# Performance work log

Hardware: AMD Instinct MI355X
Metric: run time of the kernel (lower is better)

## Reference

```python
import jax, jax.numpy as jnp
import numpy as np

B, T, C = 4, 2048, 1024
H = 16
D = C // H  # head_size = 64


def setup_inputs() -> dict:
    key = jax.random.key(0)
    ks = jax.random.split(key, 5)
    s = 0.02
    return {
        "x": jax.random.normal(ks[0], (B, T, C), dtype=jnp.float32),
        "Wq": jax.random.normal(ks[1], (C, C), dtype=jnp.float32) * s,
        "Wk": jax.random.normal(ks[2], (C, C), dtype=jnp.float32) * s,
        "Wv": jax.random.normal(ks[3], (C, C), dtype=jnp.float32) * s,
        "Wp": jax.random.normal(ks[4], (C, C), dtype=jnp.float32) * s,
        "bp": jnp.zeros((C,), dtype=jnp.float32),
    }


def reference(x, Wq, Wk, Wv, Wp, bp):
    Bq, Tq, Cq = x.shape
    # torch Linear: y = x @ W.T ; split into heads [B, H, T, D]
    def split(y):
        return y.reshape(Bq, Tq, H, D).transpose(0, 2, 1, 3)
    q = split(x @ Wq.T)
    k = split(x @ Wk.T)
    v = split(x @ Wv.T)
    # NOTE: original scales by C**-0.5 (full n_embed), not head_size**-0.5
    scale = Cq ** (-0.5)
    att = jnp.einsum('bhqd,bhkd->bhqk', q, k) * scale  # [B,H,T,T]
    causal = jnp.tril(jnp.ones((Tq, Tq), dtype=bool))
    att = jnp.where(causal[None, None, :, :], att, -jnp.inf)
    att = jax.nn.softmax(att, axis=-1)
    out = jnp.einsum('bhqk,bhkd->bhqd', att, v)  # [B,H,T,D]
    out = out.transpose(0, 2, 1, 3).reshape(Bq, Tq, Cq)
    return out @ Wp.T + bp
```

## Files before the change

kernel.cpp:

```cpp
#include <hip/hip_runtime.h>
#include <cstdint>
#include <cstddef>

typedef __attribute__((ext_vector_type(8))) __bf16 bf16x8;
typedef __attribute__((ext_vector_type(4))) __bf16 bf16x4;
typedef __attribute__((ext_vector_type(4))) float f32x4;
typedef __attribute__((ext_vector_type(16))) float f32x16;
typedef __attribute__((ext_vector_type(4))) unsigned uint4v;

#define B_ 4
#define T_ 2048
#define C_ 1024
#define H_ 16
#define D_ 64
#define NTILES_ (T_ / 32)
#define TILE_ELEMS_ 2048
#define BH_STRIDE_ ((size_t)NTILES_ * TILE_ELEMS_)

__device__ __forceinline__ float fexp2(float x) {
#if __has_builtin(__builtin_amdgcn_exp2f)
  return __builtin_amdgcn_exp2f(x);
#else
  return __expf(x * 0.69314718f);
#endif
}

__global__ __launch_bounds__(256) void castall(
    const float* __restrict__ x, const float* __restrict__ wq, const float* __restrict__ wk,
    const float* __restrict__ wv, const float* __restrict__ wp,
    __bf16* __restrict__ xb, __bf16* __restrict__ wqb, __bf16* __restrict__ wkb,
    __bf16* __restrict__ wvb, __bf16* __restrict__ wpb) {
  const int bid = blockIdx.x;
  const float* src;
  __bf16* dst;
  if (bid < 8192)       { src = x  + (size_t)bid * 1024;           dst = xb  + (size_t)bid * 1024; }
  else if (bid < 9216)  { src = wq + (size_t)(bid - 8192) * 1024;  dst = wqb + (size_t)(bid - 8192) * 1024; }
  else if (bid < 10240) { src = wk + (size_t)(bid - 9216) * 1024;  dst = wkb + (size_t)(bid - 9216) * 1024; }
  else if (bid < 11264) { src = wv + (size_t)(bid - 10240) * 1024; dst = wvb + (size_t)(bid - 10240) * 1024; }
  else                  { src = wp + (size_t)(bid - 11264) * 1024; dst = wpb + (size_t)(bid - 11264) * 1024; }
  const int i = threadIdx.x * 4;
  float4 f = *reinterpret_cast<const float4*>(src + i);
  bf16x4 o;
  o[0] = (__bf16)f.x; o[1] = (__bf16)f.y; o[2] = (__bf16)f.z; o[3] = (__bf16)f.w;
  *reinterpret_cast<bf16x4*>(dst + i) = o;
}

__device__ __forceinline__ void gload_lds16(const __bf16* g, __bf16* lds) {
  __builtin_amdgcn_global_load_lds(
      (const __attribute__((address_space(1))) void*)g,
      (__attribute__((address_space(3))) void*)lds, 16, 0, 0);
}

template <typename OUTT, bool BIAS>
__device__ __forceinline__ void gemm_bt_body(const __bf16* __restrict__ A,
                                             const __bf16* __restrict__ Bt,
                                             OUTT* __restrict__ Cp,
                                             const float* __restrict__ bias,
                                             int M, int N, int K) {
  constexpr int BK = 64;
  __shared__ __bf16 As[128 * BK];
  __shared__ __bf16 Bs[128 * BK];
  const int tid = threadIdx.x;
  const int w = tid >> 6, l = tid & 63;
  const int wr = w >> 1, wc = w & 1;
  const int lr = l & 15, lg = l >> 4;
  const int m0 = blockIdx.y * 128, n0 = blockIdx.x * 128;
  const int srow = l >> 3, scol = (l & 7) * 8;

  f32x4 acc[4][4] = {};

  for (int k0 = 0; k0 < K; k0 += BK) {
#pragma unroll
    for (int it = 0; it < 4; ++it) {
      const int c = w * 4 + it;
      gload_lds16(A + (size_t)(m0 + 8 * c + srow) * K + k0 + scol, As + c * 512);
      gload_lds16(Bt + (size_t)(n0 + 8 * c + srow) * K + k0 + scol, Bs + c * 512);
    }
    __syncthreads();
    bf16x8 af[4][2], bfv[4][2];
#pragma unroll
    for (int m = 0; m < 4; ++m)
#pragma unroll
      for (int kk = 0; kk < 2; ++kk)
        af[m][kk] = *reinterpret_cast<const bf16x8*>(As + (wr * 64 + m * 16 + lr) * BK + kk * 32 + lg * 8);
#pragma unroll
    for (int n = 0; n < 4; ++n)
#pragma unroll
      for (int kk = 0; kk < 2; ++kk)
        bfv[n][kk] = *reinterpret_cast<const bf16x8*>(Bs + (wc * 64 + n * 16 + lr) * BK + kk * 32 + lg * 8);
#pragma unroll
    for (int kk = 0; kk < 2; ++kk)
#pragma unroll
      for (int m = 0; m < 4; ++m)
#pragma unroll
        for (int n = 0; n < 4; ++n)
          acc[m][n] = __builtin_amdgcn_mfma_f32_16x16x32_bf16(af[m][kk], bfv[n][kk], acc[m][n], 0, 0, 0);
    __syncthreads();
  }
#pragma unroll
  for (int m = 0; m < 4; ++m)
#pragma unroll
    for (int n = 0; n < 4; ++n) {
      const int col = n0 + wc * 64 + n * 16 + lr;
      float bv = 0.f;
      if (BIAS) bv = bias[col];
#pragma unroll
      for (int j = 0; j < 4; ++j) {
        const int row = m0 + wr * 64 + m * 16 + lg * 4 + j;
        Cp[(size_t)row * N + col] = (OUTT)(acc[m][n][j] + bv);
      }
    }
}

__global__ __launch_bounds__(256) void gemm_proj(const __bf16* __restrict__ ao,
    const __bf16* __restrict__ wp, float* __restrict__ out, const float* __restrict__ bp) {
  gemm_bt_body<float, true>(ao, wp, out, bp, B_ * T_, C_, C_);
}

#define STAGE_A(BUFO, KT, HH)                                                         \
  do {                                                                                \
    const __bf16* s0_ = Agp + (size_t)(m0 + (HH) * 128 + srow) * 1024 + (KT) * 64 + sswz; \
    gload_lds16(s0_, LDSb + (BUFO) + (HH) * 8192 + w * 1024);                         \
    gload_lds16(s0_ + 8 * 1024, LDSb + (BUFO) + (HH) * 8192 + w * 1024 + 512);        \
  } while (0)
#define STAGE_B(BUFO, KT, HH)                                                         \
  do {                                                                                \
    const __bf16* s0_ = Bgp + (size_t)(n0 + (HH) * 128 + srow) * 1024 + (KT) * 64 + sswz; \
    gload_lds16(s0_, LDSb + 32768 + (BUFO) + (HH) * 8192 + w * 1024);                 \
    gload_lds16(s0_ + 8 * 1024, LDSb + 32768 + (BUFO) + (HH) * 8192 + w * 1024 + 512);\
  } while (0)
#define RD_A(M, KK) (*reinterpret_cast<const bf16x8*>(                                \
    LDSb + bufo + (wr * 128 + (M) * 16 + lr) * 64 + (((KK) * 32 + lg * 8) ^ ((lr & 7) * 8))))
#define RD_B(N, KK) (*reinterpret_cast<const bf16x8*>(                                \
    LDSb + 32768 + bufo + (wc * 64 + (N) * 16 + lr) * 64 + (((KK) * 32 + lg * 8) ^ ((lr & 7) * 8))))

__global__ __launch_bounds__(512, 2) void gemm_qkv8(
    const __bf16* __restrict__ Agp, const __bf16* __restrict__ Bgp,
    __bf16* __restrict__ qf, __bf16* __restrict__ kf, __bf16* __restrict__ vf) {
  __shared__ __bf16 LDSb[65536];
  const int tid = threadIdx.x;
  const int w = tid >> 6, l = tid & 63;
  const int wr = w >> 2, wc = w & 3;
  const int lr = l & 15, lg = l >> 4;
  int lin = blockIdx.y * 12 + blockIdx.x;
  lin = (lin & 7) * 48 + (lin >> 3);
  const int bx = lin % 12, by = lin / 12;
  const int m0 = by * 256, n0 = bx * 256;
  const int srow = w * 16 + (l >> 3);
  const int sswz = ((l & 7) ^ ((l >> 3) & 7)) * 8;

  f32x4 acc[8][4] = {};
  bf16x8 afl[4][2], bfl[2][2], bfh[2][2];

  STAGE_A(0, 0, 0); STAGE_A(0, 0, 1);
  STAGE_B(0, 0, 0); STAGE_B(0, 0, 1);
  __builtin_amdgcn_sched_barrier(0);
  asm volatile("s_waitcnt vmcnt(0)" ::: "memory");
  __builtin_amdgcn_s_barrier();
  __builtin_amdgcn_sched_barrier(0);

  for (int t = 0; t < 16; ++t) {
    const int bufo = (t & 1) * 16384;
    const int nbo = ((t + 1) & 1) * 16384;
    const bool st = t < 15;
#pragma unroll
    for (int m = 0; m < 4; ++m) { afl[m][0] = RD_A(m, 0); afl[m][1] = RD_A(m, 1); }
    bfl[0][0] = RD_B(0, 0); bfl[0][1] = RD_B(0, 1);
    bfl[1][0] = RD_B(1, 0); bfl[1][1] = RD_B(1, 1);
    if (st) STAGE_A(nbo, t + 1, 0);
    __builtin_amdgcn_s_setprio(1);
#pragma unroll
    for (int kk = 0; kk < 2; ++kk)
#pragma unroll
      for (int m = 0; m < 4; ++m) {
        acc[m][0] = __builtin_amdgcn_mfma_f32_16x16x32_bf16(afl[m][kk], bfl[0][kk], acc[m][0], 0, 0, 0);
        acc[m][1] = __builtin_amdgcn_mfma_f32_16x16x32_bf16(afl[m][kk], bfl[1][kk], acc[m][1], 0, 0, 0);
      }
    __builtin_amdgcn_s_setprio(0);
    __builtin_amdgcn_s_barrier();
    bfh[0][0] = RD_B(2, 0); bfh[0][1] = RD_B(2, 1);
    bfh[1][0] = RD_B(3, 0); bfh[1][1] = RD_B(3, 1);
    if (st) STAGE_A(nbo, t + 1, 1);
    __builtin_amdgcn_s_setprio(1);
#pragma unroll
    for (int kk = 0; kk < 2; ++kk)
#pragma unroll
      for (int m = 0; m < 4; ++m) {
        acc[m][2] = __builtin_amdgcn_mfma_f32_16x16x32_bf16(afl[m][kk], bfh[0][kk], acc[m][2], 0, 0, 0);
        acc[m][3] = __builtin_amdgcn_mfma_f32_16x16x32_bf16(afl[m][kk], bfh[1][kk], acc[m][3], 0, 0, 0);
      }
    __builtin_amdgcn_s_setprio(0);
    __builtin_amdgcn_s_barrier();
#pragma unroll
    for (int m = 0; m < 4; ++m) { afl[m][0] = RD_A(m + 4, 0); afl[m][1] = RD_A(m + 4, 1); }
    if (st) STAGE_B(nbo, t + 1, 0);
    __builtin_amdgcn_s_setprio(1);
#pragma unroll
    for (int kk = 0; kk < 2; ++kk)
#pragma unroll
      for (int m = 0; m < 4; ++m) {
        acc[m + 4][0] = __builtin_amdgcn_mfma_f32_16x16x32_bf16(afl[m][kk], bfl[0][kk], acc[m + 4][0], 0, 0, 0);
        acc[m + 4][1] = __builtin_amdgcn_mfma_f32_16x16x32_bf16(afl[m][kk], bfl[1][kk], acc[m + 4][1], 0, 0, 0);
      }
    __builtin_amdgcn_s_setprio(0);
    __builtin_amdgcn_s_barrier();
    if (st) STAGE_B(nbo, t + 1, 1);
    __builtin_amdgcn_s_setprio(1);
#pragma unroll
    for (int kk = 0; kk < 2; ++kk)
#pragma unroll
      for (int m = 0; m < 4; ++m) {
        acc[m + 4][2] = __builtin_amdgcn_mfma_f32_16x16x32_bf16(afl[m][kk], bfh[0][kk], acc[m + 4][2], 0, 0, 0);
        acc[m + 4][3] = __builtin_amdgcn_mfma_f32_16x16x32_bf16(afl[m][kk], bfh[1][kk], acc[m + 4][3], 0, 0, 0);
      }
    __builtin_amdgcn_s_setprio(0);
    __builtin_amdgcn_sched_barrier(0);
    asm volatile("s_waitcnt vmcnt(0)" ::: "memory");
    __builtin_amdgcn_s_barrier();
    __builtin_amdgcn_sched_barrier(0);
  }

  __bf16* wl = LDSb + w * 8192;
  const int colb = n0 + wc * 64;
  const int mat = colb >> 10;
  const int h = (colb >> 6) & 15;
  const int b = m0 >> 11;
  const float qsc = (mat == 0) ? 0.04508422f : 1.0f;
#pragma unroll
  for (int m = 0; m < 8; ++m) {
    const int rt = m >> 1;
#pragma unroll
    for (int n = 0; n < 4; ++n) {
      const int d = n * 16 + lr;
#pragma unroll
      for (int j = 0; j < 4; ++j) {
        const int rowloc = (m & 1) * 16 + lg * 4 + j;
        int off;
        if (mat < 2)
          off = ((d >> 4) & 3) * 512 + ((d >> 3) & 1) * 256 + rowloc * 8 + (d & 7);
        else
          off = (d >> 5) * 1024 + ((rowloc >> 4) & 1) * 512 + ((rowloc >> 3) & 1) * 256 +
                (d & 31) * 8 + (rowloc & 7);
        wl[rt * 2048 + off] = (__bf16)(acc[m][n][j] * qsc);
      }
    }
  }
  __bf16* dstbase = (mat == 0 ? qf : mat == 1 ? kf : vf) + (size_t)(b * 16 + h) * BH_STRIDE_;
  const int rt0 = ((m0 + wr * 128) >> 5) & 63;
#pragma unroll
  for (int rt = 0; rt < 4; ++rt)
#pragma unroll
    for (int c = 0; c < 4; ++c) {
      const bf16x8 vchunk = *reinterpret_cast<const bf16x8*>(wl + rt * 2048 + c * 512 + l * 8);
      *reinterpret_cast<bf16x8*>(dstbase + (size_t)(rt0 + rt) * TILE_ELEMS_ + c * 512 + l * 8) = vchunk;
    }
}

__device__ __forceinline__ unsigned pk2(float a, float b) {
  const unsigned short ua = __builtin_bit_cast(unsigned short, (__bf16)a);
  const unsigned short ub = __builtin_bit_cast(unsigned short, (__bf16)b);
  return (unsigned)ua | ((unsigned)ub << 16);
}

#define LOADKV(SFX, TT)                                                          \
  do {                                                                           \
    const __bf16* kp_ = kfb + (size_t)(TT) * TILE_ELEMS_ + lx8;                  \
    k##SFX##0 = *reinterpret_cast<const bf16x8*>(kp_);                           \
    k##SFX##1 = *reinterpret_cast<const bf16x8*>(kp_ + 512);                     \
    k##SFX##2 = *reinterpret_cast<const bf16x8*>(kp_ + 1024);                    \
    k##SFX##3 = *reinterpret_cast<const bf16x8*>(kp_ + 1536);                    \
    const __bf16* vp_ = vfb + (size_t)(TT) * TILE_ELEMS_ + lx8;                  \
    v##SFX##0 = *reinterpret_cast<const bf16x8*>(vp_);                           \
    v##SFX##1 = *reinterpret_cast<const bf16x8*>(vp_ + 512);                     \
    v##SFX##2 = *reinterpret_cast<const bf16x8*>(vp_ + 1024);                    \
    v##SFX##3 = *reinterpret_cast<const bf16x8*>(vp_ + 1536);                    \
  } while (0)

#define TILE(SFX, MASKED)                                                        \
  do {                                                                           \
    f32x16 s = {};                                                               \
    __builtin_amdgcn_s_setprio(1);                                               \
    s = __builtin_amdgcn_mfma_f32_32x32x16_bf16(k##SFX##0, qf[0], s, 0, 0, 0);   \
    s = __builtin_amdgcn_mfma_f32_32x32x16_bf16(k##SFX##1, qf[1], s, 0, 0, 0);   \
    s = __builtin_amdgcn_mfma_f32_32x32x16_bf16(k##SFX##2, qf[2], s, 0, 0, 0);   \
    s = __builtin_amdgcn_mfma_f32_32x32x16_bf16(k##SFX##3, qf[3], s, 0, 0, 0);   \
    __builtin_amdgcn_s_setprio(0);                                               \
    float sv[16];                                                                \
    _Pragma("unroll") for (int r = 0; r < 16; ++r) sv[r] = s[r];                 \
    if (MASKED) {                                                                \
      _Pragma("unroll") for (int r = 0; r < 16; ++r) {                           \
        const int kvloc = (r & 3) + 8 * (r >> 2) + 4 * hi;                       \
        sv[r] = (kvloc <= lane31) ? sv[r] : -1e30f;                              \
      }                                                                          \
    }                                                                            \
    _Pragma("unroll") for (int r = 0; r < 16; ++r) sv[r] = fexp2(sv[r]);         \
    unsigned pwv[8];                                                             \
    _Pragma("unroll") for (int ks = 0; ks < 2; ++ks) {                           \
      const unsigned X0 = pk2(sv[ks * 8 + 0], sv[ks * 8 + 1]);                   \
      const unsigned X1 = pk2(sv[ks * 8 + 2], sv[ks * 8 + 3]);                   \
      const unsigned Y0 = pk2(sv[ks * 8 + 4], sv[ks * 8 + 5]);                   \
      const unsigned Y1 = pk2(sv[ks * 8 + 6], sv[ks * 8 + 7]);                   \
      const unsigned sX0 = __shfl_xor(X0, 32);                                   \
      const unsigned sX1 = __shfl_xor(X1, 32);                                   \
      const unsigned sY0 = __shfl_xor(Y0, 32);                                   \
      const unsigned sY1 = __shfl_xor(Y1, 32);                                   \
      pwv[ks * 4 + 0] = hi ? sY0 : X0;                                           \
      pwv[ks * 4 + 1] = hi ? sY1 : X1;                                           \
      pwv[ks * 4 + 2] = hi ? Y0 : sX0;                                           \
      pwv[ks * 4 + 3] = hi ? Y1 : sX1;                                           \
    }                                                                            \
    const uint4v u0 = {pwv[0], pwv[1], pwv[2], pwv[3]};                          \
    const uint4v u1 = {pwv[4], pwv[5], pwv[6], pwv[7]};                          \
    const bf16x8 pf0 = __builtin_bit_cast(bf16x8, u0);                           \
    const bf16x8 pf1 = __builtin_bit_cast(bf16x8, u1);                           \
    __builtin_amdgcn_s_setprio(1);                                               \
    acc0 = __builtin_amdgcn_mfma_f32_32x32x16_bf16(v##SFX##0, pf0, acc0, 0, 0, 0); \
    acc0 = __builtin_amdgcn_mfma_f32_32x32x16_bf16(v##SFX##1, pf1, acc0, 0, 0, 0); \
    acc1 = __builtin_amdgcn_mfma_f32_32x32x16_bf16(v##SFX##2, pf0, acc1, 0, 0, 0); \
    acc1 = __builtin_amdgcn_mfma_f32_32x32x16_bf16(v##SFX##3, pf1, acc1, 0, 0, 0); \
    __builtin_amdgcn_s_setprio(0);                                               \
    float b8[8];                                                                 \
    _Pragma("unroll") for (int r = 0; r < 8; ++r) b8[r] = sv[2 * r] + sv[2 * r + 1]; \
    _Pragma("unroll") for (int r = 0; r < 4; ++r) b8[r] = b8[2 * r] + b8[2 * r + 1]; \
    l_run += (b8[0] + b8[1]) + (b8[2] + b8[3]);                                  \
  } while (0)

__global__ __launch_bounds__(512) void attn_fwd(const __bf16* __restrict__ qfr,
                                                const __bf16* __restrict__ kfr,
                                                const __bf16* __restrict__ vfr,
                                                __bf16* __restrict__ ao) {
  __shared__ float Pls[4 * 64 * 34];
  const int tid = threadIdx.x;
  const int w = tid >> 6, l = tid & 63;
  const int p = w >> 1, hf = w & 1;
  const int lane31 = l & 31, hi = l >> 5;
  const int bh = blockIdx.y;
  const int b = bh >> 4;
  const int qx = blockIdx.x * 4 + p;
  const size_t rowbase = (size_t)b * T_;
  const int hoff = (bh & 15) * D_;
  const int lx8 = l * 8;
  const __bf16* qfb = qfr + (size_t)bh * BH_STRIDE_;
  const __bf16* kfb = kfr + (size_t)bh * BH_STRIDE_;
  const __bf16* vfb = vfr + (size_t)bh * BH_STRIDE_;
  float* pb = Pls + p * (64 * 34) + l * 34;

  for (int phase = 0; phase < 2; ++phase) {
    const int qg = (phase ? 63 - qx : qx) * 32;
    const int ntiles = (qg >> 5) + 1;
    const int nh = ntiles >> 1;
    const int tb = hf ? nh : 0;
    const int te = hf ? ntiles : nh;
    const int nt = te - tb;
    const bool dm = (hf == 1);

    bf16x8 qf[4];
    {
      const __bf16* qp = qfb + (size_t)(qg >> 5) * TILE_ELEMS_ + lx8;
#pragma unroll
      for (int t4 = 0; t4 < 4; ++t4) qf[t4] = *reinterpret_cast<const bf16x8*>(qp + t4 * 512);
    }

    f32x16 acc0 = {};
    f32x16 acc1 = {};
    float l_run = 0.f;

    bf16x8 kA0, kA1, kA2, kA3, vA0, vA1, vA2, vA3;
    bf16x8 kB0, kB1, kB2, kB3, vB0, vB1, vB2, vB3;

    if (nt > 0) {
      LOADKV(A, tb);
      int i = 0;
      for (; i + 1 < nt; ++i) {
        if ((i & 1) == 0) { LOADKV(B, tb + i + 1); TILE(A, false); }
        else              { LOADKV(A, tb + i + 1); TILE(B, false); }
      }
      if ((i & 1) == 0) TILE(A, dm);
      else              TILE(B, dm);
    }

    if (hf) {
#pragma unroll
      for (int r = 0; r < 16; ++r) { pb[r] = acc0[r]; pb[16 + r] = acc1[r]; }
      pb[32] = l_run;
    }
    __syncthreads();
    if (!hf) {
#pragma unroll
      for (int r = 0; r < 16; ++r) { acc0[r] += pb[r]; acc1[r] += pb[16 + r]; }
      l_run += pb[32];
      l_run += __shfl_xor(l_run, 32);
      const float rl = 1.0f / l_run;
      __bf16* op = ao + (rowbase + qg + lane31) * C_ + hoff + hi * 4;
#pragma unroll
      for (int dblk = 0; dblk < 2; ++dblk)
#pragma unroll
        for (int qd = 0; qd < 4; ++qd) {
          bf16x4 ov;
#pragma unroll
          for (int j = 0; j < 4; ++j) {
            const float av = (dblk == 0) ? acc0[qd * 4 + j] : acc1[qd * 4 + j];
            ov[j] = (__bf16)(av * rl);
          }
          *reinterpret_cast<bf16x4*>(op + dblk * 32 + qd * 8) = ov;
        }
    }
    __syncthreads();
  }
}

extern "C" void kernel_launch(void* const* d_in, const int* in_sizes, int n_in,
                              void* d_out, int out_size, void* d_ws, size_t ws_size,
                              hipStream_t stream) {
  const float* x  = (const float*)d_in[0];
  const float* Wq = (const float*)d_in[1];
  const float* Wk = (const float*)d_in[2];
  const float* Wv = (const float*)d_in[3];
  const float* Wp = (const float*)d_in[4];
  const float* bp = (const float*)d_in[5];
  float* out = (float*)d_out;

  const int NX = B_ * T_ * C_;
  const int NW = C_ * C_;

  __bf16* xb  = (__bf16*)d_ws;
  __bf16* wqb = xb + NX;
  __bf16* wkb = wqb + NW;
  __bf16* wvb = wkb + NW;
  __bf16* wpb = wvb + NW;
  __bf16* qf  = wpb + NW;
  __bf16* kf  = qf + NX;
  __bf16* vf  = kf + NX;
  __bf16* aob = xb;

  castall<<<12288, 256, 0, stream>>>(x, Wq, Wk, Wv, Wp, xb, wqb, wkb, wvb, wpb);

  gemm_qkv8<<<dim3(12, 32), 512, 0, stream>>>(xb, wqb, qf, kf, vf);
  attn_fwd<<<dim3(8, B_ * H_), 512, 0, stream>>>(qf, kf, vf, aob);
  gemm_proj<<<dim3(C_ / 128, (B_ * T_) / 128), 256, 0, stream>>>(aob, wpb, out, bp);
}
```

Measured before the change: 181.5 us.

## Reuse pipelined 256x256 GEMM kernel for output projection and remap attention grid

Pulls the double-buffered, swizzled 256x256-tile k-loop of the QKV GEMM into a shared macro. A new gemm_proj8 kernel built on it replaces the simple 128x128 projection GEMM and adds the bias in its epilogue. The attention launch becomes a 1D grid with the head index in the low bits, which changes which blocks run together and so their cache locality. The projection now runs only 128 blocks of 512 threads, which may under-fill the GPU's compute units.

```diff
diff --git a/kernel.cpp b/kernel.cpp
--- a/kernel.cpp
+++ b/kernel.cpp
@@ -51,72 +51,6 @@
       (__attribute__((address_space(3))) void*)lds, 16, 0, 0);
 }
 
-template <typename OUTT, bool BIAS>
-__device__ __forceinline__ void gemm_bt_body(const __bf16* __restrict__ A,
-                                             const __bf16* __restrict__ Bt,
-                                             OUTT* __restrict__ Cp,
-                                             const float* __restrict__ bias,
-                                             int M, int N, int K) {
-  constexpr int BK = 64;
-  __shared__ __bf16 As[128 * BK];
-  __shared__ __bf16 Bs[128 * BK];
-  const int tid = threadIdx.x;
-  const int w = tid >> 6, l = tid & 63;
-  const int wr = w >> 1, wc = w & 1;
-  const int lr = l & 15, lg = l >> 4;
-  const int m0 = blockIdx.y * 128, n0 = blockIdx.x * 128;
-  const int srow = l >> 3, scol = (l & 7) * 8;
-
-  f32x4 acc[4][4] = {};
-
-  for (int k0 = 0; k0 < K; k0 += BK) {
-#pragma unroll
-    for (int it = 0; it < 4; ++it) {
-      const int c = w * 4 + it;
-      gload_lds16(A + (size_t)(m0 + 8 * c + srow) * K + k0 + scol, As + c * 512);
-      gload_lds16(Bt + (size_t)(n0 + 8 * c + srow) * K + k0 + scol, Bs + c * 512);
-    }
-    __syncthreads();
-    bf16x8 af[4][2], bfv[4][2];
-#pragma unroll
-    for (int m = 0; m < 4; ++m)
-#pragma unroll
-      for (int kk = 0; kk < 2; ++kk)
-        af[m][kk] = *reinterpret_cast<const bf16x8*>(As + (wr * 64 + m * 16 + lr) * BK + kk * 32 + lg * 8);
-#pragma unroll
-    for (int n = 0; n < 4; ++n)
-#pragma unroll
-      for (int kk = 0; kk < 2; ++kk)
-        bfv[n][kk] = *reinterpret_cast<const bf16x8*>(Bs + (wc * 64 + n * 16 + lr) * BK + kk * 32 + lg * 8);
-#pragma unroll
-    for (int kk = 0; kk < 2; ++kk)
-#pragma unroll
-      for (int m = 0; m < 4; ++m)
-#pragma unroll
-        for (int n = 0; n < 4; ++n)
-          acc[m][n] = __builtin_amdgcn_mfma_f32_16x16x32_bf16(af[m][kk], bfv[n][kk], acc[m][n], 0, 0, 0);
-    __syncthreads();
-  }
-#pragma unroll
-  for (int m = 0; m < 4; ++m)
-#pragma unroll
-    for (int n = 0; n < 4; ++n) {
-      const int col = n0 + wc * 64 + n * 16 + lr;
-      float bv = 0.f;
-      if (BIAS) bv = bias[col];
-#pragma unroll
-      for (int j = 0; j < 4; ++j) {
-        const int row = m0 + wr * 64 + m * 16 + lg * 4 + j;
-        Cp[(size_t)row * N + col] = (OUTT)(acc[m][n][j] + bv);
-      }
-    }
-}
-
-__global__ __launch_bounds__(256) void gemm_proj(const __bf16* __restrict__ ao,
-    const __bf16* __restrict__ wp, float* __restrict__ out, const float* __restrict__ bp) {
-  gemm_bt_body<float, true>(ao, wp, out, bp, B_ * T_, C_, C_);
-}
-
 #define STAGE_A(BUFO, KT, HH)                                                         \
   do {                                                                                \
     const __bf16* s0_ = Agp + (size_t)(m0 + (HH) * 128 + srow) * 1024 + (KT) * 64 + sswz; \
@@ -134,6 +68,74 @@
 #define RD_B(N, KK) (*reinterpret_cast<const bf16x8*>(                                \
     LDSb + 32768 + bufo + (wc * 64 + (N) * 16 + lr) * 64 + (((KK) * 32 + lg * 8) ^ ((lr & 7) * 8))))
 
+#define GEMM8_KLOOP                                                                   \
+  STAGE_A(0, 0, 0); STAGE_A(0, 0, 1);                                                 \
+  STAGE_B(0, 0, 0); STAGE_B(0, 0, 1);                                                 \
+  __builtin_amdgcn_sched_barrier(0);                                                  \
+  asm volatile("s_waitcnt vmcnt(0)" ::: "memory");                                    \
+  __builtin_amdgcn_s_barrier();                                                       \
+  __builtin_amdgcn_sched_barrier(0);                                                  \
+  for (int t = 0; t < 16; ++t) {                                                      \
+    const int bufo = (t & 1) * 16384;                                                 \
+    const int nbo = ((t + 1) & 1) * 16384;                                            \
+    const bool st = t < 15;                                                           \
+    _Pragma("unroll")                                                                 \
+    for (int m = 0; m < 4; ++m) { afl[m][0] = RD_A(m, 0); afl[m][1] = RD_A(m, 1); }   \
+    bfl[0][0] = RD_B(0, 0); bfl[0][1] = RD_B(0, 1);                                   \
+    bfl[1][0] = RD_B(1, 0); bfl[1][1] = RD_B(1, 1);                                   \
+    if (st) STAGE_A(nbo, t + 1, 0);                                                   \
+    __builtin_amdgcn_s_setprio(1);                                                    \
+    _Pragma("unroll")                                                                 \
+    for (int kk = 0; kk < 2; ++kk)                                                    \
+      _Pragma("unroll")                                                               \
+      for (int m = 0; m < 4; ++m) {                                                   \
+        acc[m][0] = __builtin_amdgcn_mfma_f32_16x16x32_bf16(afl[m][kk], bfl[0][kk], acc[m][0], 0, 0, 0); \
+        acc[m][1] = __builtin_amdgcn_mfma_f32_16x16x32_bf16(afl[m][kk], bfl[1][kk], acc[m][1], 0, 0, 0); \
+      }                                                                               \
+    __builtin_amdgcn_s_setprio(0);                                                    \
+    __builtin_amdgcn_s_barrier();                                                     \
+    bfh[0][0] = RD_B(2, 0); bfh[0][1] = RD_B(2, 1);                                   \
+    bfh[1][0] = RD_B(3, 0); bfh[1][1] = RD_B(3, 1);                                   \
+    if (st) STAGE_A(nbo, t + 1, 1);                                                   \
+    __builtin_amdgcn_s_setprio(1);                                                    \
+    _Pragma("unroll")                                                                 \
+    for (int kk = 0; kk < 2; ++kk)                                                    \
+      _Pragma("unroll")                                                               \
+      for (int m = 0; m < 4; ++m) {                                                   \
+        acc[m][2] = __builtin_amdgcn_mfma_f32_16x16x32_bf16(afl[m][kk], bfh[0][kk], acc[m][2], 0, 0, 0); \
+        acc[m][3] = __builtin_amdgcn_mfma_f32_16x16x32_bf16(afl[m][kk], bfh[1][kk], acc[m][3], 0, 0, 0); \
+      }                                                                               \
+    __builtin_amdgcn_s_setprio(0);                                                    \
+    __builtin_amdgcn_s_barrier();                                                     \
+    _Pragma("unroll")                                                                 \
+    for (int m = 0; m < 4; ++m) { afl[m][0] = RD_A(m + 4, 0); afl[m][1] = RD_A(m + 4, 1); } \
+    if (st) STAGE_B(nbo, t + 1, 0);                                                   \
+    __builtin_amdgcn_s_setprio(1);                                                    \
+    _Pragma("unroll")                                                                 \
+    for (int kk = 0; kk < 2; ++kk)                                                    \
+      _Pragma("unroll")                                                               \
+      for (int m = 0; m < 4; ++m) {                                                   \
+        acc[m + 4][0] = __builtin_amdgcn_mfma_f32_16x16x32_bf16(afl[m][kk], bfl[0][kk], acc[m + 4][0], 0, 0, 0); \
+        acc[m + 4][1] = __builtin_amdgcn_mfma_f32_16x16x32_bf16(afl[m][kk], bfl[1][kk], acc[m + 4][1], 0, 0, 0); \
+      }                                                                               \
+    __builtin_amdgcn_s_setprio(0);                                                    \
+    __builtin_amdgcn_s_barrier();                                                     \
+    if (st) STAGE_B(nbo, t + 1, 1);                                                   \
+    __builtin_amdgcn_s_setprio(1);                                                    \
+    _Pragma("unroll")                                                                 \
+    for (int kk = 0; kk < 2; ++kk)                                                    \
+      _Pragma("unroll")                                                               \
+      for (int m = 0; m < 4; ++m) {                                                   \
+        acc[m + 4][2] = __builtin_amdgcn_mfma_f32_16x16x32_bf16(afl[m][kk], bfh[0][kk], acc[m + 4][2], 0, 0, 0); \
+        acc[m + 4][3] = __builtin_amdgcn_mfma_f32_16x16x32_bf16(afl[m][kk], bfh[1][kk], acc[m + 4][3], 0, 0, 0); \
+      }                                                                               \
+    __builtin_amdgcn_s_setprio(0);                                                    \
+    __builtin_amdgcn_sched_barrier(0);                                                \
+    asm volatile("s_waitcnt vmcnt(0)" ::: "memory");                                  \
+    __builtin_amdgcn_s_barrier();                                                     \
+    __builtin_amdgcn_sched_barrier(0);                                                \
+  }
+
 __global__ __launch_bounds__(512, 2) void gemm_qkv8(
     const __bf16* __restrict__ Agp, const __bf16* __restrict__ Bgp,
     __bf16* __restrict__ qf, __bf16* __restrict__ kf, __bf16* __restrict__ vf) {
@@ -152,73 +154,7 @@
   f32x4 acc[8][4] = {};
   bf16x8 afl[4][2], bfl[2][2], bfh[2][2];
 
-  STAGE_A(0, 0, 0); STAGE_A(0, 0, 1);
-  STAGE_B(0, 0, 0); STAGE_B(0, 0, 1);
-  __builtin_amdgcn_sched_barrier(0);
-  asm volatile("s_waitcnt vmcnt(0)" ::: "memory");
-  __builtin_amdgcn_s_barrier();
-  __builtin_amdgcn_sched_barrier(0);
-
-  for (int t = 0; t < 16; ++t) {
-    const int bufo = (t & 1) * 16384;
-    const int nbo = ((t + 1) & 1) * 16384;
-    const bool st = t < 15;
-#pragma unroll
-    for (int m = 0; m < 4; ++m) { afl[m][0] = RD_A(m, 0); afl[m][1] = RD_A(m, 1); }
-    bfl[0][0] = RD_B(0, 0); bfl[0][1] = RD_B(0, 1);
-    bfl[1][0] = RD_B(1, 0); bfl[1][1] = RD_B(1, 1);
-    if (st) STAGE_A(nbo, t + 1, 0);
-    __builtin_amdgcn_s_setprio(1);
-#pragma unroll
-    for (int kk = 0; kk < 2; ++kk)
-#pragma unroll
-      for (int m = 0; m < 4; ++m) {
-        acc[m][0] = __builtin_amdgcn_mfma_f32_16x16x32_bf16(afl[m][kk], bfl[0][kk], acc[m][0], 0, 0, 0);
-        acc[m][1] = __builtin_amdgcn_mfma_f32_16x16x32_bf16(afl[m][kk], bfl[1][kk], acc[m][1], 0, 0, 0);
-      }
-    __builtin_amdgcn_s_setprio(0);
-    __builtin_amdgcn_s_barrier();
-    bfh[0][0] = RD_B(2, 0); bfh[0][1] = RD_B(2, 1);
-    bfh[1][0] = RD_B(3, 0); bfh[1][1] = RD_B(3, 1);
-    if (st) STAGE_A(nbo, t + 1, 1);
-    __builtin_amdgcn_s_setprio(1);
-#pragma unroll
-    for (int kk = 0; kk < 2; ++kk)
-#pragma unroll
-      for (int m = 0; m < 4; ++m) {
-        acc[m][2] = __builtin_amdgcn_mfma_f32_16x16x32_bf16(afl[m][kk], bfh[0][kk], acc[m][2], 0, 0, 0);
-        acc[m][3] = __builtin_amdgcn_mfma_f32_16x16x32_bf16(afl[m][kk], bfh[1][kk], acc[m][3], 0, 0, 0);
-      }
-    __builtin_amdgcn_s_setprio(0);
-    __builtin_amdgcn_s_barrier();
-#pragma unroll
-    for (int m = 0; m < 4; ++m) { afl[m][0] = RD_A(m + 4, 0); afl[m][1] = RD_A(m + 4, 1); }
-    if (st) STAGE_B(nbo, t + 1, 0);
-    __builtin_amdgcn_s_setprio(1);
-#pragma unroll
-    for (int kk = 0; kk < 2; ++kk)
-#pragma unroll
-      for (int m = 0; m < 4; ++m) {
-        acc[m + 4][0] = __builtin_amdgcn_mfma_f32_16x16x32_bf16(afl[m][kk], bfl[0][kk], acc[m + 4][0], 0, 0, 0);
-        acc[m + 4][1] = __builtin_amdgcn_mfma_f32_16x16x32_bf16(afl[m][kk], bfl[1][kk], acc[m + 4][1], 0, 0, 0);
-      }
-    __builtin_amdgcn_s_setprio(0);
-    __builtin_amdgcn_s_barrier();
-    if (st) STAGE_B(nbo, t + 1, 1);
-    __builtin_amdgcn_s_setprio(1);
-#pragma unroll
-    for (int kk = 0; kk < 2; ++kk)
-#pragma unroll
-      for (int m = 0; m < 4; ++m) {
-        acc[m + 4][2] = __builtin_amdgcn_mfma_f32_16x16x32_bf16(afl[m][kk], bfh[0][kk], acc[m + 4][2], 0, 0, 0);
-        acc[m + 4][3] = __builtin_amdgcn_mfma_f32_16x16x32_bf16(afl[m][kk], bfh[1][kk], acc[m + 4][3], 0, 0, 0);
-      }
-    __builtin_amdgcn_s_setprio(0);
-    __builtin_amdgcn_sched_barrier(0);
-    asm volatile("s_waitcnt vmcnt(0)" ::: "memory");
-    __builtin_amdgcn_s_barrier();
-    __builtin_amdgcn_sched_barrier(0);
-  }
+  GEMM8_KLOOP
 
   __bf16* wl = LDSb + w * 8192;
   const int colb = n0 + wc * 64;
@@ -254,6 +190,41 @@
       const bf16x8 vchunk = *reinterpret_cast<const bf16x8*>(wl + rt * 2048 + c * 512 + l * 8);
       *reinterpret_cast<bf16x8*>(dstbase + (size_t)(rt0 + rt) * TILE_ELEMS_ + c * 512 + l * 8) = vchunk;
     }
+}
+
+__global__ __launch_bounds__(512, 2) void gemm_proj8(
+    const __bf16* __restrict__ Agp, const __bf16* __restrict__ Bgp,
+    float* __restrict__ out, const float* __restrict__ bias) {
+  __shared__ __bf16 LDSb[65536];
+  const int tid = threadIdx.x;
+  const int w = tid >> 6, l = tid & 63;
+  const int wr = w >> 2, wc = w & 3;
+  const int lr = l & 15, lg = l >> 4;
+  int lin = blockIdx.y * 4 + blockIdx.x;
+  lin = (lin & 7) * 16 + (lin >> 3);
+  const int bx = lin & 3, by = lin >> 2;
+  const int m0 = by * 256, n0 = bx * 256;
+  const int srow = w * 16 + (l >> 3);
+  const int sswz = ((l & 7) ^ ((l >> 3) & 7)) * 8;
+
+  f32x4 acc[8][4] = {};
+  bf16x8 afl[4][2], bfl[2][2], bfh[2][2];
+
+  GEMM8_KLOOP
+
+  const int colb = n0 + wc * 64;
+#pragma unroll
+  for (int m = 0; m < 8; ++m) {
+    const int row = m0 + wr * 128 + (m >> 1) * 32 + (m & 1) * 16 + lg * 4;
+#pragma unroll
+    for (int n = 0; n < 4; ++n) {
+      const int col = colb + n * 16 + lr;
+      const float bv = bias[col];
+#pragma unroll
+      for (int j = 0; j < 4; ++j)
+        out[(size_t)(row + j) * 1024 + col] = acc[m][n][j] + bv;
+    }
+  }
 }
 
 __device__ __forceinline__ unsigned pk2(float a, float b) {
@@ -334,9 +305,10 @@
   const int w = tid >> 6, l = tid & 63;
   const int p = w >> 1, hf = w & 1;
   const int lane31 = l & 31, hi = l >> 5;
-  const int bh = blockIdx.y;
+  const int bh = blockIdx.x & 63;
+  const int qi = blockIdx.x >> 6;
   const int b = bh >> 4;
-  const int qx = blockIdx.x * 4 + p;
+  const int qx = qi * 4 + p;
   const size_t rowbase = (size_t)b * T_;
   const int hoff = (bh & 15) * D_;
   const int lx8 = l * 8;
@@ -436,6 +408,6 @@
   castall<<<12288, 256, 0, stream>>>(x, Wq, Wk, Wv, Wp, xb, wqb, wkb, wvb, wpb);
 
   gemm_qkv8<<<dim3(12, 32), 512, 0, stream>>>(xb, wqb, qf, kf, vf);
-  attn_fwd<<<dim3(8, B_ * H_), 512, 0, stream>>>(qf, kf, vf, aob);
-  gemm_proj<<<dim3(C_ / 128, (B_ * T_) / 128), 256, 0, stream>>>(aob, wpb, out, bp);
-}
+  attn_fwd<<<512, 512, 0, stream>>>(qf, kf, vf, aob);
+  gemm_proj8<<<dim3(4, 32), 512, 0, stream>>>(aob, wpb, out, bp);
+}
```

Result: faster. 172.0 us (-5.2%).
